# Performance work log

Measured on AMD Instinct MI355X. Metric: run time of the kernel, lower is better.

The kernel has to match this reference:

```python
import jax, jax.numpy as jnp
import numpy as np

N1 = 100000  # source cloud size (x1)
N2 = 100000  # target cloud size (x2)
F = 64       # point feature dim
E = 1600000  # number of radius edges (avg 16 neighbors)
H = 128      # MLP hidden/out dim


def setup_inputs() -> dict:
    key = jax.random.key(0)
    ks = jax.random.split(key, 12)
    s = 0.05
    return {
        "x1_features": jax.random.normal(ks[0], (N1, F), jnp.float32),
        "x1_pos": jax.random.normal(ks[1], (N1, 3), jnp.float32),
        "x2_features": jax.random.normal(ks[2], (N2, F), jnp.float32),
        "x2_pos": jax.random.normal(ks[3], (N2, 3), jnp.float32),
        "W1": jax.random.normal(ks[4], (2 * F + 3, H), jnp.float32) * s,
        "b1": jnp.zeros((H,), jnp.float32),
        "W2": jax.random.normal(ks[5], (H, H), jnp.float32) * s,
        "b2": jnp.zeros((H,), jnp.float32),
        "W3": jax.random.normal(ks[6], (H, H), jnp.float32) * s,
        "b3": jnp.zeros((H,), jnp.float32),
        "edge_src": jax.random.randint(ks[7], (E,), 0, N1, jnp.int32),
        "edge_dst": jax.random.randint(ks[8], (E,), 0, N2, jnp.int32),
    }


def reference(x1_features, x1_pos, x2_features, x2_pos,
              W1, b1, W2, b2, W3, b3, edge_src, edge_dst):
    # message(x_i, x_j, pos_i, pos_j): i = target (x2, edge_dst), j = source (x1, edge_src)
    # msg = cat([x_i, x_j, pos_j - pos_i], dim=1)  -> [E, 2F+3]
    msg = jnp.concatenate(
        [x2_features[edge_dst],
         x1_features[edge_src],
         x1_pos[edge_src] - x2_pos[edge_dst]], axis=1)
    # MLP (Linear+ReLU x3, FastFlow3D make_mlp style)
    h = jax.nn.relu(msg @ W1 + b1)
    h = jax.nn.relu(h @ W2 + b2)
    h = jax.nn.relu(h @ W3 + b3)
    # scatter-max aggregation onto x2 nodes; PyG fills empty segments with 0
    out = jax.ops.segment_max(h, edge_dst, num_segments=N2)
    out = jnp.where(jnp.isneginf(out), 0.0, out)
    return out, x2_pos
```

## Files before the change

kernel.cpp:

```cpp
#include <hip/hip_runtime.h>
#include <hip/hip_bf16.h>

#define DEV __device__ __forceinline__

typedef short bf16x8 __attribute__((ext_vector_type(8)));
typedef float f32x16 __attribute__((ext_vector_type(16)));

static constexpr int FDIM  = 64;
static constexpr int HH    = 128;
static constexpr int K1RAW = 2 * FDIM + 3;
static constexpr int K1    = 144;
static constexpr int KS1   = K1 / 16;
static constexpr int KS2   = HH / 16;
static constexpr int TM    = 128;

static constexpr int MSTR  = 2 * K1;
static constexpr int HSTR  = 2 * HH;
static constexpr int L_MSG = 0;
static constexpr int L_H   = TM * MSTR;
static constexpr int L_DST = L_H + TM * HSTR;
static constexpr int L_TOT = L_DST + TM * 4;

static constexpr int WT1_ELEMS = HH * K1;
static constexpr int WT2_ELEMS = HH * HH;
static constexpr int WT_TOTAL  = WT1_ELEMS + 2 * WT2_ELEMS;

DEV unsigned pack2(float a, float b) {
    union { __hip_bfloat162 h; unsigned u; } cv;
    cv.h.x = __float2bfloat16(a);
    cv.h.y = __float2bfloat16(b);
    return cv.u;
}
DEV unsigned short f2bf(float f) {
    union { __hip_bfloat16 h; unsigned short u; } cv;
    cv.h = __float2bfloat16(f);
    return cv.u;
}
DEV int swz_msg(int c, int r) { const int m = (c < 16) ? 7 : 1; return (c & ~m) | ((c ^ r) & m); }
DEV int swz_h(int c, int r)   { return (c & ~7) | ((c ^ r) & 7); }

__global__ void k_cvt(const float* __restrict__ src, unsigned short* __restrict__ dst, int n8) {
    int i = blockIdx.x * 256 + threadIdx.x;
    if (i < n8) {
        float4 a = *(const float4*)(src + (size_t)i * 8);
        float4 b = *(const float4*)(src + (size_t)i * 8 + 4);
        uint4 o;
        o.x = pack2(a.x, a.y); o.y = pack2(a.z, a.w);
        o.z = pack2(b.x, b.y); o.w = pack2(b.z, b.w);
        *(uint4*)(dst + (size_t)i * 8) = o;
    }
}

__global__ void k_wprep(const float* __restrict__ W1, const float* __restrict__ W2,
                        const float* __restrict__ W3, unsigned short* __restrict__ wt) {
    int i = blockIdx.x * 256 + threadIdx.x;
    if (i < WT1_ELEMS) {
        int n = i / K1, k = i % K1;
        float v = (k < K1RAW) ? W1[k * HH + n] : 0.f;
        wt[i] = f2bf(v);
    } else if (i < WT1_ELEMS + WT2_ELEMS) {
        int j = i - WT1_ELEMS; int n = j / HH, k = j % HH;
        wt[i] = f2bf(W2[k * HH + n]);
    } else if (i < WT_TOTAL) {
        int j = i - WT1_ELEMS - WT2_ELEMS; int n = j / HH, k = j % HH;
        wt[i] = f2bf(W3[k * HH + n]);
    }
}

__global__ void k_hist(const int* __restrict__ edst, int* __restrict__ cnt, int E) {
    int e = blockIdx.x * 256 + threadIdx.x;
    if (e < E) atomicAdd(&cnt[edst[e]], 1);
}

__global__ void k_scan_part(const int* __restrict__ cnt, int* __restrict__ partial, int n2) {
    __shared__ int sm[256];
    int t = threadIdx.x;
    int base = blockIdx.x * 1024 + t * 4;
    int s = 0;
#pragma unroll
    for (int j = 0; j < 4; j++) { int idx = base + j; if (idx < n2) s += cnt[idx]; }
    sm[t] = s; __syncthreads();
    for (int off = 128; off > 0; off >>= 1) {
        if (t < off) sm[t] += sm[t + off];
        __syncthreads();
    }
    if (t == 0) partial[blockIdx.x] = sm[0];
}

__global__ void k_scan_top(int* __restrict__ partial, int nb) {
    __shared__ int sm[256];
    int t = threadIdx.x;
    int v = (t < nb) ? partial[t] : 0;
    sm[t] = v; __syncthreads();
    for (int off = 1; off < 256; off <<= 1) {
        int add = (t >= off) ? sm[t - off] : 0;
        __syncthreads();
        sm[t] += add;
        __syncthreads();
    }
    if (t < nb) partial[t] = sm[t] - v;
}

__global__ void k_scan_down(const int* __restrict__ cnt, const int* __restrict__ partial,
                            int* __restrict__ cursor, int n2) {
    __shared__ int sm[256];
    int t = threadIdx.x;
    int base = blockIdx.x * 1024 + t * 4;
    int c[4]; int s = 0;
#pragma unroll
    for (int j = 0; j < 4; j++) { int idx = base + j; c[j] = (idx < n2) ? cnt[idx] : 0; s += c[j]; }
    sm[t] = s; __syncthreads();
    for (int off = 1; off < 256; off <<= 1) {
        int add = (t >= off) ? sm[t - off] : 0;
        __syncthreads();
        sm[t] += add;
        __syncthreads();
    }
    int run = partial[blockIdx.x] + (sm[t] - s);
#pragma unroll
    for (int j = 0; j < 4; j++) {
        int idx = base + j;
        if (idx < n2) cursor[idx] = run;
        run += c[j];
    }
}

__global__ void k_fill(const int* __restrict__ edst, int* __restrict__ cursor,
                       int* __restrict__ csr_e, int* __restrict__ csr_d, int E) {
    int e = blockIdx.x * 256 + threadIdx.x;
    if (e < E) {
        int d = edst[e];
        int p = atomicAdd(&cursor[d], 1);
        csr_e[p] = e;
        csr_d[p] = d;
    }
}

DEV f32x16 zerov() {
    f32x16 v;
#pragma unroll
    for (int i = 0; i < 16; i++) v[i] = 0.f;
    return v;
}

template <int STRIDE>
DEV void tile_store(const f32x16& acc, const float* __restrict__ bias, char* __restrict__ hb,
                    int rt, int ct, int l31, int hh) {
    const int r = ct * 32 + l31;
#pragma unroll
    for (int g = 0; g < 4; g++) {
        float4 bv = *(const float4*)(bias + rt * 32 + 8 * g + 4 * hh);
        float v0 = fmaxf(acc[4 * g + 0] + bv.x, 0.f);
        float v1 = fmaxf(acc[4 * g + 1] + bv.y, 0.f);
        float v2 = fmaxf(acc[4 * g + 2] + bv.z, 0.f);
        float v3 = fmaxf(acc[4 * g + 3] + bv.w, 0.f);
        uint2 w; w.x = pack2(v0, v1); w.y = pack2(v2, v3);
        *(uint2*)(hb + r * STRIDE + swz_h(4 * rt + g, r) * 16 + 8 * hh) = w;
    }
}

template <int KSTEPS, int STRIDE, bool MSG, int OSTRIDE>
DEV void layer(const unsigned short* __restrict__ wtl, const char* __restrict__ src,
               const float* __restrict__ bias, char* __restrict__ dst,
               int rt, int ct0, int l31, int hh) {
    bf16x8 A[KSTEPS];
#pragma unroll
    for (int ks = 0; ks < KSTEPS; ks++)
        A[ks] = *(const bf16x8*)(wtl + (rt * 32 + l31) * (KSTEPS * 16) + ks * 16 + 8 * hh);
#pragma unroll
    for (int j = 0; j < 2; j++) {
        const int r = (ct0 + j) * 32 + l31;
        bf16x8 B[KSTEPS];
#pragma unroll
        for (int ks = 0; ks < KSTEPS; ks++) {
            const int c = 2 * ks + hh;
            const int cs = MSG ? swz_msg(c, r) : swz_h(c, r);
            B[ks] = *(const bf16x8*)(src + r * STRIDE + cs * 16);
        }
        f32x16 acc = zerov();
#pragma unroll
        for (int ks = 0; ks < KSTEPS; ks++)
            acc = __builtin_amdgcn_mfma_f32_32x32x16_bf16(A[ks], B[ks], acc, 0, 0, 0);
        tile_store<OSTRIDE>(acc, bias, dst, rt, ct0 + j, l31, hh);
    }
}

template <bool SORTED, bool BF16SRC>
__global__ __launch_bounds__(512, 4) void k_main(
    const float* __restrict__ x1f, const float* __restrict__ x1p,
    const float* __restrict__ x2f, const float* __restrict__ x2p,
    const char* __restrict__ xb1, const char* __restrict__ xb2,
    const float* __restrict__ b1, const float* __restrict__ b2, const float* __restrict__ b3,
    const unsigned short* __restrict__ wt,
    const int* __restrict__ csr_e, const int* __restrict__ csr_d,
    const int* __restrict__ edge_src, const int* __restrict__ edge_dst,
    float* __restrict__ out, int E) {
    __shared__ __align__(16) char sm[L_TOT];
    char* msg = sm + L_MSG;
    char* hbf = sm + L_H;
    int*  dl  = (int*)(sm + L_DST);

    const int tid  = threadIdx.x;
    const int lane = tid & 63;
    const int wv   = tid >> 6;
    const int l31  = lane & 31;
    const int hh   = lane >> 5;
    const int eb   = blockIdx.x * TM;

    {
        const int r   = tid >> 2;
        const int sub = tid & 3;
        const int slot = eb + r;
        const bool ok = slot < E;
        int e = 0, d = 0, s = 0;
        if (ok) {
            if (SORTED) { e = csr_e[slot]; d = csr_d[slot]; }
            else        { e = slot;        d = edge_dst[e]; }
            s = edge_src[e];
        }
        if (sub == 0) dl[r] = ok ? d : -1;
        char* row = msg + r * MSTR;
        const int c0 = sub * 4;
#pragma unroll
        for (int i = 0; i < 4; i++) {
            const int c = c0 + i;
            uint4 v; v.x = v.y = v.z = v.w = 0u;
            if (ok) {
                const int cc = c & 7;
                if (BF16SRC) {
                    const char* base = (c < 8) ? (xb2 + (size_t)d * (2 * FDIM))
                                               : (xb1 + (size_t)s * (2 * FDIM));
                    v = *(const uint4*)(base + cc * 16);
                } else {
                    const float* base = (c < 8) ? (x2f + (size_t)d * FDIM)
                                                : (x1f + (size_t)s * FDIM);
                    float4 a = *(const float4*)(base + cc * 8);
                    float4 b = *(const float4*)(base + cc * 8 + 4);
                    v.x = pack2(a.x, a.y); v.y = pack2(a.z, a.w);
                    v.z = pack2(b.x, b.y); v.w = pack2(b.z, b.w);
                }
            }
            *(uint4*)(row + swz_msg(c, r) * 16) = v;
        }
        if (sub == 3) {
            float dx = 0.f, dy = 0.f, dz = 0.f;
            if (ok) {
                dx = x1p[s * 3 + 0] - x2p[d * 3 + 0];
                dy = x1p[s * 3 + 1] - x2p[d * 3 + 1];
                dz = x1p[s * 3 + 2] - x2p[d * 3 + 2];
            }
            uint4 v; v.x = pack2(dx, dy); v.y = pack2(dz, 0.f); v.z = 0u; v.w = 0u;
            *(uint4*)(row + swz_msg(16, r) * 16) = v;
            uint4 z; z.x = z.y = z.z = z.w = 0u;
            *(uint4*)(row + swz_msg(17, r) * 16) = z;
        }
    }
    __syncthreads();

    const int rt  = wv & 3;
    const int ct0 = (wv >> 2) * 2;

    layer<KS1, MSTR, true, HSTR>(wt, msg, b1, hbf, rt, ct0, l31, hh);
    __syncthreads();
    layer<KS2, HSTR, false, MSTR>(wt + WT1_ELEMS, hbf, b2, msg, rt, ct0, l31, hh);
    __syncthreads();
    layer<KS2, MSTR, false, HSTR>(wt + WT1_ELEMS + WT2_ELEMS, msg, b3, hbf, rt, ct0, l31, hh);
    __syncthreads();

    {
        const int feat  = tid & 127;
        const int strip = tid >> 7;
        const int r0 = strip * 32;
        int curd = dl[r0];
        int rs = r0;
        float m = 0.f;
#pragma unroll
        for (int b = 0; b < 4; b++) {
            float vals[8];
            int   ds[8];
#pragma unroll
            for (int j = 0; j < 8; j++) {
                const int r = r0 + b * 8 + j;
                unsigned short w = *(const unsigned short*)(
                    hbf + r * HSTR + swz_h(feat >> 3, r) * 16 + (feat & 7) * 2);
                vals[j] = __uint_as_float(((unsigned)w) << 16);
                ds[j]   = dl[r];
            }
#pragma unroll
            for (int j = 0; j < 8; j++) {
                const int r = r0 + b * 8 + j;
                const int d = ds[j];
                if (d != curd) {
                    if (curd >= 0) {
                        bool extL = (rs == r0) && (r0 == 0 || dl[r0 - 1] == curd);
                        if (extL) {
                            if (m > 0.f)
                                atomicMax((int*)out + (size_t)curd * HH + feat, __float_as_int(m));
                        } else {
                            out[(size_t)curd * HH + feat] = m;
                        }
                    }
                    curd = d; rs = r; m = 0.f;
                }
                m = fmaxf(m, vals[j]);
            }
        }
        if (curd >= 0) {
            bool extL = (rs == r0) && (r0 == 0 || dl[r0 - 1] == curd);
            bool extR = (r0 + 32 == TM) || (dl[r0 + 32] == curd);
            if (extL || extR) {
                if (m > 0.f)
                    atomicMax((int*)out + (size_t)curd * HH + feat, __float_as_int(m));
            } else {
                out[(size_t)curd * HH + feat] = m;
            }
        }
    }
}

extern "C" void kernel_launch(void* const* d_in, const int* in_sizes, int n_in,
                              void* d_out, int out_size, void* d_ws, size_t ws_size,
                              hipStream_t stream) {
    const float* x1f = (const float*)d_in[0];
    const float* x1p = (const float*)d_in[1];
    const float* x2f = (const float*)d_in[2];
    const float* x2p = (const float*)d_in[3];
    const float* W1  = (const float*)d_in[4];
    const float* b1  = (const float*)d_in[5];
    const float* W2  = (const float*)d_in[6];
    const float* b2  = (const float*)d_in[7];
    const float* W3  = (const float*)d_in[8];
    const float* b3  = (const float*)d_in[9];
    const int* esrc  = (const int*)d_in[10];
    const int* edst  = (const int*)d_in[11];
    const int E  = in_sizes[10];
    const int N1 = in_sizes[1] / 3;
    const int N2 = in_sizes[3] / 3;
    float* out = (float*)d_out;

    size_t off = 0;
    auto take = [&](size_t bytes) { size_t o = off; off = (off + bytes + 255) & ~(size_t)255; return o; };
    size_t o_cnt = take(4 * (size_t)N2);
    size_t o_cur = take(4 * (size_t)N2);
    size_t o_par = take(4 * 256);
    size_t o_ce  = take(4 * (size_t)E);
    size_t o_cd  = take(4 * (size_t)E);
    size_t o_wt  = take(2 * (size_t)WT_TOTAL);
    size_t need_csr = off;
    size_t o_x1  = take(2 * (size_t)N1 * FDIM);
    size_t o_x2  = take(2 * (size_t)N2 * FDIM);
    size_t need_bf = off;

    const int NB = (N2 + 1023) / 1024;
    bool use_csr = (need_csr <= ws_size) && (NB <= 256);
    bool use_bf  = (need_bf <= ws_size);

    char* ws = (char*)d_ws;
    unsigned short* wt = use_csr ? (unsigned short*)(ws + o_wt) : (unsigned short*)ws;
    int* cnt    = (int*)(ws + o_cnt);
    int* cursor = (int*)(ws + o_cur);
    int* part   = (int*)(ws + o_par);
    int* csr_e  = (int*)(ws + o_ce);
    int* csr_d  = (int*)(ws + o_cd);
    char* xb1   = ws + o_x1;
    char* xb2   = ws + o_x2;

    (void)hipMemsetAsync(out, 0, (size_t)N2 * HH * 4, stream);
    (void)hipMemcpyAsync(out + (size_t)N2 * HH, x2p, (size_t)N2 * 3 * 4,
                         hipMemcpyDeviceToDevice, stream);

    k_wprep<<<(WT_TOTAL + 255) / 256, 256, 0, stream>>>(W1, W2, W3, wt);

    if (use_bf) {
        int n8_1 = N1 * FDIM / 8, n8_2 = N2 * FDIM / 8;
        k_cvt<<<(n8_1 + 255) / 256, 256, 0, stream>>>(x1f, (unsigned short*)xb1, n8_1);
        k_cvt<<<(n8_2 + 255) / 256, 256, 0, stream>>>(x2f, (unsigned short*)xb2, n8_2);
    }

    const int grid = (E + TM - 1) / TM;
    if (use_csr) {
        (void)hipMemsetAsync(cnt, 0, 4 * (size_t)N2, stream);
        k_hist<<<(E + 255) / 256, 256, 0, stream>>>(edst, cnt, E);
        k_scan_part<<<NB, 256, 0, stream>>>(cnt, part, N2);
        k_scan_top<<<1, 256, 0, stream>>>(part, NB);
        k_scan_down<<<NB, 256, 0, stream>>>(cnt, part, cursor, N2);
        k_fill<<<(E + 255) / 256, 256, 0, stream>>>(edst, cursor, csr_e, csr_d, E);
        if (use_bf)
            k_main<true, true><<<grid, 512, 0, stream>>>(
                x1f, x1p, x2f, x2p, xb1, xb2, b1, b2, b3, wt, csr_e, csr_d, esrc, edst, out, E);
        else
            k_main<true, false><<<grid, 512, 0, stream>>>(
                x1f, x1p, x2f, x2p, xb1, xb2, b1, b2, b3, wt, csr_e, csr_d, esrc, edst, out, E);
    } else {
        if (use_bf)
            k_main<false, true><<<grid, 512, 0, stream>>>(
                x1f, x1p, x2f, x2p, xb1, xb2, b1, b2, b3, wt, edst, edst, esrc, edst, out, E);
        else
            k_main<false, false><<<grid, 512, 0, stream>>>(
                x1f, x1p, x2f, x2p, xb1, xb2, b1, b2, b3, wt, edst, edst, esrc, edst, out, E);
    }
}
```

Measured before the change: 596.7 us.

## Switch LDS tiles to column-chunk-major layout with padded stride, rework segment-max reduction

Replaces the row-major, XOR-swizzled shared-memory layout for message and hidden tiles with a chunk-major layout: each 16-byte feature chunk is stored as a column across all 128 rows, with a padded chunk stride. MFMA operand loads and tile stores become simple strided addresses with no swizzle arithmetic. The scatter-max epilogue now has each thread handle two adjacent features over 16-row strips, reading packed 32-bit words. This aims to cut address computation and LDS bank conflicts, but splitting rows into smaller strips can raise the number of boundary atomics.

Result: no change. 597.9 us (+0.2%).

```diff
diff --git a/kernel.cpp b/kernel.cpp
--- a/kernel.cpp
+++ b/kernel.cpp
@@ -14,11 +14,12 @@
 static constexpr int KS2   = HH / 16;
 static constexpr int TM    = 128;
 
-static constexpr int MSTR  = 2 * K1;
-static constexpr int HSTR  = 2 * HH;
+static constexpr int CSTR  = TM * 16 + 16;
+static constexpr int MCH   = 18;
+static constexpr int HCH   = 16;
 static constexpr int L_MSG = 0;
-static constexpr int L_H   = TM * MSTR;
-static constexpr int L_DST = L_H + TM * HSTR;
+static constexpr int L_H   = MCH * CSTR;
+static constexpr int L_DST = L_H + HCH * CSTR;
 static constexpr int L_TOT = L_DST + TM * 4;
 
 static constexpr int WT1_ELEMS = HH * K1;
@@ -36,8 +37,6 @@
     cv.h = __float2bfloat16(f);
     return cv.u;
 }
-DEV int swz_msg(int c, int r) { const int m = (c < 16) ? 7 : 1; return (c & ~m) | ((c ^ r) & m); }
-DEV int swz_h(int c, int r)   { return (c & ~7) | ((c ^ r) & 7); }
 
 __global__ void k_cvt(const float* __restrict__ src, unsigned short* __restrict__ dst, int n8) {
     int i = blockIdx.x * 256 + threadIdx.x;
@@ -143,10 +142,26 @@
     return v;
 }
 
-template <int STRIDE>
-DEV void tile_store(const f32x16& acc, const float* __restrict__ bias, char* __restrict__ hb,
-                    int rt, int ct, int l31, int hh) {
-    const int r = ct * 32 + l31;
+template <int KSTEPS>
+DEV void load_A(const unsigned short* __restrict__ wtl, int rt, int l31, int hh, bf16x8* A) {
+#pragma unroll
+    for (int ks = 0; ks < KSTEPS; ks++)
+        A[ks] = *(const bf16x8*)(wtl + (rt * 32 + l31) * (KSTEPS * 16) + ks * 16 + 8 * hh);
+}
+
+template <int KSTEPS>
+DEV f32x16 tile_mfma(const bf16x8* A, const char* __restrict__ srcrow) {
+    f32x16 acc = zerov();
+#pragma unroll
+    for (int ks = 0; ks < KSTEPS; ks++) {
+        bf16x8 B = *(const bf16x8*)(srcrow + 2 * ks * CSTR);
+        acc = __builtin_amdgcn_mfma_f32_32x32x16_bf16(A[ks], B, acc, 0, 0, 0);
+    }
+    return acc;
+}
+
+DEV void tile_store(const f32x16& acc, const float* __restrict__ bias, char* __restrict__ dstrow,
+                    int rt, int hh) {
 #pragma unroll
     for (int g = 0; g < 4; g++) {
         float4 bv = *(const float4*)(bias + rt * 32 + 8 * g + 4 * hh);
@@ -155,33 +170,7 @@
         float v2 = fmaxf(acc[4 * g + 2] + bv.z, 0.f);
         float v3 = fmaxf(acc[4 * g + 3] + bv.w, 0.f);
         uint2 w; w.x = pack2(v0, v1); w.y = pack2(v2, v3);
-        *(uint2*)(hb + r * STRIDE + swz_h(4 * rt + g, r) * 16 + 8 * hh) = w;
-    }
-}
-
-template <int KSTEPS, int STRIDE, bool MSG, int OSTRIDE>
-DEV void layer(const unsigned short* __restrict__ wtl, const char* __restrict__ src,
-               const float* __restrict__ bias, char* __restrict__ dst,
-               int rt, int ct0, int l31, int hh) {
-    bf16x8 A[KSTEPS];
-#pragma unroll
-    for (int ks = 0; ks < KSTEPS; ks++)
-        A[ks] = *(const bf16x8*)(wtl + (rt * 32 + l31) * (KSTEPS * 16) + ks * 16 + 8 * hh);
-#pragma unroll
-    for (int j = 0; j < 2; j++) {
-        const int r = (ct0 + j) * 32 + l31;
-        bf16x8 B[KSTEPS];
-#pragma unroll
-        for (int ks = 0; ks < KSTEPS; ks++) {
-            const int c = 2 * ks + hh;
-            const int cs = MSG ? swz_msg(c, r) : swz_h(c, r);
-            B[ks] = *(const bf16x8*)(src + r * STRIDE + cs * 16);
-        }
-        f32x16 acc = zerov();
-#pragma unroll
-        for (int ks = 0; ks < KSTEPS; ks++)
-            acc = __builtin_amdgcn_mfma_f32_32x32x16_bf16(A[ks], B[ks], acc, 0, 0, 0);
-        tile_store<OSTRIDE>(acc, bias, dst, rt, ct0 + j, l31, hh);
+        *(uint2*)(dstrow + g * CSTR) = w;
     }
 }
 
@@ -219,11 +208,10 @@
             s = edge_src[e];
         }
         if (sub == 0) dl[r] = ok ? d : -1;
-        char* row = msg + r * MSTR;
-        const int c0 = sub * 4;
+        char* colbase = msg + r * 16 + (sub * 4) * CSTR;
 #pragma unroll
         for (int i = 0; i < 4; i++) {
-            const int c = c0 + i;
+            const int c = sub * 4 + i;
             uint4 v; v.x = v.y = v.z = v.w = 0u;
             if (ok) {
                 const int cc = c & 7;
@@ -240,7 +228,7 @@
                     v.z = pack2(b.x, b.y); v.w = pack2(b.z, b.w);
                 }
             }
-            *(uint4*)(row + swz_msg(c, r) * 16) = v;
+            *(uint4*)(colbase + i * CSTR) = v;
         }
         if (sub == 3) {
             float dx = 0.f, dy = 0.f, dz = 0.f;
@@ -249,70 +237,83 @@
                 dy = x1p[s * 3 + 1] - x2p[d * 3 + 1];
                 dz = x1p[s * 3 + 2] - x2p[d * 3 + 2];
             }
+            char* rowb = msg + r * 16;
             uint4 v; v.x = pack2(dx, dy); v.y = pack2(dz, 0.f); v.z = 0u; v.w = 0u;
-            *(uint4*)(row + swz_msg(16, r) * 16) = v;
+            *(uint4*)(rowb + 16 * CSTR) = v;
             uint4 z; z.x = z.y = z.z = z.w = 0u;
-            *(uint4*)(row + swz_msg(17, r) * 16) = z;
+            *(uint4*)(rowb + 17 * CSTR) = z;
         }
     }
     __syncthreads();
 
     const int rt  = wv & 3;
     const int ct0 = (wv >> 2) * 2;
-
-    layer<KS1, MSTR, true, HSTR>(wt, msg, b1, hbf, rt, ct0, l31, hh);
+    bf16x8 A[KS1];
+
+    load_A<KS1>(wt, rt, l31, hh, A);
+#pragma unroll
+    for (int j = 0; j < 2; j++) {
+        const int r = (ct0 + j) * 32 + l31;
+        f32x16 acc = tile_mfma<KS1>(A, msg + r * 16 + hh * CSTR);
+        tile_store(acc, b1, hbf + r * 16 + 8 * hh + (4 * rt) * CSTR, rt, hh);
+    }
     __syncthreads();
-    layer<KS2, HSTR, false, MSTR>(wt + WT1_ELEMS, hbf, b2, msg, rt, ct0, l31, hh);
+
+    load_A<KS2>(wt + WT1_ELEMS, rt, l31, hh, A);
+#pragma unroll
+    for (int j = 0; j < 2; j++) {
+        const int r = (ct0 + j) * 32 + l31;
+        f32x16 acc = tile_mfma<KS2>(A, hbf + r * 16 + hh * CSTR);
+        tile_store(acc, b2, msg + r * 16 + 8 * hh + (4 * rt) * CSTR, rt, hh);
+    }
     __syncthreads();
-    layer<KS2, MSTR, false, HSTR>(wt + WT1_ELEMS + WT2_ELEMS, msg, b3, hbf, rt, ct0, l31, hh);
+
+    load_A<KS2>(wt + WT1_ELEMS + WT2_ELEMS, rt, l31, hh, A);
+#pragma unroll
+    for (int j = 0; j < 2; j++) {
+        const int r = (ct0 + j) * 32 + l31;
+        f32x16 acc = tile_mfma<KS2>(A, msg + r * 16 + hh * CSTR);
+        tile_store(acc, b3, hbf + r * 16 + 8 * hh + (4 * rt) * CSTR, rt, hh);
+    }
     __syncthreads();
 
     {
-        const int feat  = tid & 127;
-        const int strip = tid >> 7;
-        const int r0 = strip * 32;
+        const int p     = tid & 63;
+        const int strip = tid >> 6;
+        const int r0 = strip * 16;
+        const char* fbase = hbf + (p >> 2) * CSTR + (p & 3) * 4;
         int curd = dl[r0];
         int rs = r0;
-        float m = 0.f;
-#pragma unroll
-        for (int b = 0; b < 4; b++) {
-            float vals[8];
-            int   ds[8];
-#pragma unroll
-            for (int j = 0; j < 8; j++) {
-                const int r = r0 + b * 8 + j;
-                unsigned short w = *(const unsigned short*)(
-                    hbf + r * HSTR + swz_h(feat >> 3, r) * 16 + (feat & 7) * 2);
-                vals[j] = __uint_as_float(((unsigned)w) << 16);
-                ds[j]   = dl[r];
+        float m0 = 0.f, m1 = 0.f;
+#pragma unroll
+        for (int r = r0; r < r0 + 16; r++) {
+            int d = dl[r];
+            if (d != curd) {
+                if (curd >= 0) {
+                    bool extL = (rs == r0) && (r0 == 0 || dl[r0 - 1] == curd);
+                    if (extL) {
+                        if (m0 > 0.f) atomicMax((int*)out + (size_t)curd * HH + 2 * p,     __float_as_int(m0));
+                        if (m1 > 0.f) atomicMax((int*)out + (size_t)curd * HH + 2 * p + 1, __float_as_int(m1));
+                    } else {
+                        out[(size_t)curd * HH + 2 * p]     = m0;
+                        out[(size_t)curd * HH + 2 * p + 1] = m1;
+                    }
+                }
+                curd = d; rs = r; m0 = 0.f; m1 = 0.f;
             }
-#pragma unroll
-            for (int j = 0; j < 8; j++) {
-                const int r = r0 + b * 8 + j;
-                const int d = ds[j];
-                if (d != curd) {
-                    if (curd >= 0) {
-                        bool extL = (rs == r0) && (r0 == 0 || dl[r0 - 1] == curd);
-                        if (extL) {
-                            if (m > 0.f)
-                                atomicMax((int*)out + (size_t)curd * HH + feat, __float_as_int(m));
-                        } else {
-                            out[(size_t)curd * HH + feat] = m;
-                        }
-                    }
-                    curd = d; rs = r; m = 0.f;
-                }
-                m = fmaxf(m, vals[j]);
-            }
+            unsigned w = *(const unsigned*)(fbase + r * 16);
+            m0 = fmaxf(m0, __uint_as_float(w << 16));
+            m1 = fmaxf(m1, __uint_as_float(w & 0xffff0000u));
         }
         if (curd >= 0) {
             bool extL = (rs == r0) && (r0 == 0 || dl[r0 - 1] == curd);
-            bool extR = (r0 + 32 == TM) || (dl[r0 + 32] == curd);
+            bool extR = (r0 + 16 == TM) || (dl[r0 + 16] == curd);
             if (extL || extR) {
-                if (m > 0.f)
-                    atomicMax((int*)out + (size_t)curd * HH + feat, __float_as_int(m));
+                if (m0 > 0.f) atomicMax((int*)out + (size_t)curd * HH + 2 * p,     __float_as_int(m0));
+                if (m1 > 0.f) atomicMax((int*)out + (size_t)curd * HH + 2 * p + 1, __float_as_int(m1));
             } else {
-                out[(size_t)curd * HH + feat] = m;
+                out[(size_t)curd * HH + 2 * p]     = m0;
+                out[(size_t)curd * HH + 2 * p + 1] = m1;
             }
         }
     }
```
